# Optimization experiments

Hardware: AMD Instinct MI355X
Metric: run time of the kernel (lower is better)

## Reference

```python
import jax, jax.numpy as jnp
import numpy as np

N = 262144          # batch size
C = 100             # num_classes
R0, R1 = 0.95, 1.0  # recall_range
LAM = 0.5           # lambda_pauc
LS = 0.1            # label_smoothing
MAX_PAUC = R1 - R0


def setup_inputs() -> dict:
    key = jax.random.key(0)
    k1, k2 = jax.random.split(key)
    predictions = jax.random.normal(k1, (N, C), dtype=jnp.float32)
    targets = jax.random.randint(k2, (N,), 0, C)
    weight = jnp.ones((C,), dtype=jnp.float32)
    return {"predictions": predictions, "targets": targets, "weight": weight}


def _roc_curves(scores, labels):
    """Vectorized per-class ROC. scores, labels: [C, N].
    Replaces the O(N^2) per-threshold loop with sort + cumsum (tie-correct:
    tp at threshold s_j counts ALL samples with score >= s_j)."""
    order = jnp.argsort(-scores, axis=1)                      # descending
    ss = jnp.take_along_axis(scores, order, axis=1)           # [C, N]
    sl = jnp.take_along_axis(labels, order, axis=1)           # [C, N]
    cpos = jnp.cumsum(sl, axis=1)                             # cumulative positives
    # last index within each tie-group of equal scores
    neg = -ss  # ascending
    idx = jax.vmap(lambda a: jnp.searchsorted(a, a, side='right'))(neg) - 1
    tp = jnp.take_along_axis(cpos, idx, axis=1)
    cnt = (idx + 1).astype(scores.dtype)
    fp = cnt - tp
    P = cpos[:, -1:]                       # total positives per class
    Nn = scores.shape[1] - P               # total negatives per class
    tpr = jnp.where(P > 0, tp / jnp.maximum(P, 1.0), 0.0)
    fpr = jnp.where(Nn > 0, fp / jnp.maximum(Nn, 1.0), 0.0)
    return fpr, tpr


def reference(predictions, targets, weight):
    probs = jax.nn.softmax(predictions, axis=1)               # [N, C]
    onehot = jnp.eye(C, dtype=predictions.dtype)[targets]     # [N, C]
    onehot_s = (1.0 - LS) * onehot + LS / C

    # per-class binary labels (smoothed true-class value > 0.5)
    labels = (onehot_s > 0.5).astype(predictions.dtype).T     # [C, N]
    scores = probs.T                                          # [C, N]

    fpr, tpr = _roc_curves(scores, labels)
    mask = (tpr >= R0) & (tpr <= R1)
    y = jnp.maximum(tpr - R0, 0.0)
    # tpr is monotone non-decreasing, so the recall mask is contiguous and
    # trapz over the masked subset == sum over adjacent pairs both in mask.
    pm = (mask[:, :-1] & mask[:, 1:]).astype(predictions.dtype)
    pauc = jnp.sum(0.5 * (y[:, :-1] + y[:, 1:]) * (fpr[:, 1:] - fpr[:, :-1]) * pm, axis=1)  # [C]

    avg_p_auc = jnp.sum(pauc * weight) / (jnp.sum(weight) * MAX_PAUC)
    # torch computes TP/FP via .item(): the pAUC path carries no gradient
    avg_p_auc = jax.lax.stop_gradient(jnp.clip(avg_p_auc, 0.0, 1.0))

    log_probs = jax.nn.log_softmax(predictions, axis=1)
    ce_loss = -jnp.mean(jnp.sum(onehot_s * log_probs * weight, axis=1))
    pauc_loss = 1.0 - avg_p_auc ** 2
    return (1.0 - LAM) * ce_loss + LAM * pauc_loss
```

## Files before the change

### kernel.cpp

```cpp
#include <hip/hip_runtime.h>
#include <math.h>

#define WAVE 64
constexpr int   CC      = 100;
constexpr int   MAXM    = 160;
constexpr int   BUCKET  = 4096;
constexpr int   USTRIDE = 161;
constexpr int   LCAP    = 2048;
constexpr float LSMOOTH = 0.1f;
constexpr int   TILE    = 64;
constexpr int   T4TILE  = TILE * CC / 4;
constexpr int   K3AGRID = 1024;
constexpr int   K3BGRID = 128;

__device__ __forceinline__ void gload_lds16(const void* g, void* lds) {
    __builtin_amdgcn_global_load_lds(
        (const __attribute__((address_space(1))) void*)g,
        (__attribute__((address_space(3))) void*)lds, 16, 0, 0);
}

__global__ __launch_bounds__(256) void k1_tile(
    const float* __restrict__ pred, const int* __restrict__ targets,
    const float* __restrict__ weight, float* __restrict__ L_out,
    float* __restrict__ pos_out, float* __restrict__ ce_partial, int N)
{
    __shared__ float tile[TILE * CC];
    __shared__ int   ttgt[TILE];
    __shared__ float tL[TILE], tpos[TILE];
    __shared__ float cered[4];
    const int tid = threadIdx.x;
    const int r0  = blockIdx.x * TILE;

    const float4* src = (const float4*)(pred + (size_t)r0 * CC);
    {
        int t = tid;
        #pragma unroll
        for (int k = 0; k < T4TILE / 256; ++k) {
            gload_lds16((const void*)(src + t), (char*)tile + (size_t)t * 16);
            t += 256;
        }
        if (t < T4TILE)
            gload_lds16((const void*)(src + t), (char*)tile + (size_t)t * 16);
    }
    if (tid < TILE) ttgt[tid] = targets[r0 + tid];
    asm volatile("s_waitcnt vmcnt(0)" ::: "memory");
    __syncthreads();

    const int x = tid & 15;
    const int G = tid >> 4;
    float w[7];
    #pragma unroll
    for (int j = 0; j < 7; ++j) {
        int c = x + 16 * j;
        w[j] = (c < CC) ? weight[c] : 0.0f;
    }
    float Wl = 0.0f;
    #pragma unroll
    for (int j = 0; j < 7; ++j) Wl += w[j];
    #pragma unroll
    for (int off = 1; off < 16; off <<= 1) Wl += __shfl_xor(Wl, off, 16);

    float ce_acc = 0.0f;
    #pragma unroll
    for (int rr = 0; rr < 4; ++rr) {
        const int r = G * 4 + rr;
        const float* rp = tile + r * CC;
        float v[7];
        #pragma unroll
        for (int j = 0; j < 7; ++j) {
            int c = x + 16 * j;
            v[j] = (c < CC) ? rp[c] : -INFINITY;
        }
        float vmax = v[0];
        #pragma unroll
        for (int j = 1; j < 7; ++j) vmax = fmaxf(vmax, v[j]);
        #pragma unroll
        for (int off = 1; off < 16; off <<= 1) vmax = fmaxf(vmax, __shfl_xor(vmax, off, 16));
        float z = 0.0f, ws = 0.0f;
        #pragma unroll
        for (int j = 0; j < 7; ++j) {
            int c = x + 16 * j;
            if (c < CC) { z += __expf(v[j] - vmax); ws += w[j] * v[j]; }
        }
        #pragma unroll
        for (int off = 1; off < 16; off <<= 1) {
            z  += __shfl_xor(z,  off, 16);
            ws += __shfl_xor(ws, off, 16);
        }
        float L = vmax + __logf(z);
        if (x == 0) {
            int t = ttgt[r];
            float pt = rp[t];
            tL[r] = L; tpos[r] = pt - L;
            ce_acc += -((1.0f - LSMOOTH) * weight[t] * (pt - L)
                        + (LSMOOTH / CC) * (ws - Wl * L));
        }
    }
    #pragma unroll
    for (int off = 32; off; off >>= 1) ce_acc += __shfl_xor(ce_acc, off, WAVE);
    if ((tid & 63) == 0) cered[tid >> 6] = ce_acc;
    __syncthreads();
    if (tid < TILE) {
        L_out[r0 + tid]   = tL[tid];
        pos_out[r0 + tid] = tpos[tid];
    }
    if (tid == 0)
        ce_partial[blockIdx.x] = cered[0] + cered[1] + cered[2] + cered[3];
}

__global__ __launch_bounds__(256) void k1b_scatter(
    const int* __restrict__ targets, const float* __restrict__ pos,
    int* __restrict__ cls_cnt, float* __restrict__ bucket, int N)
{
    __shared__ int hist[CC];
    __shared__ int base[CC];
    __shared__ int loc[CC];
    const int tid = threadIdx.x;
    const int rowsPerBlock = N / gridDim.x;
    const int r0 = blockIdx.x * rowsPerBlock;
    const int r1 = r0 + rowsPerBlock;
    for (int c = tid; c < CC; c += blockDim.x) { hist[c] = 0; loc[c] = 0; }
    __syncthreads();
    for (int r = r0 + tid; r < r1; r += blockDim.x)
        atomicAdd(&hist[targets[r]], 1);
    __syncthreads();
    for (int c = tid; c < CC; c += blockDim.x)
        base[c] = (hist[c] > 0) ? atomicAdd(&cls_cnt[c], hist[c]) : 0;
    __syncthreads();
    for (int r = r0 + tid; r < r1; r += blockDim.x) {
        int c = targets[r];
        int idx = base[c] + atomicAdd(&loc[c], 1);
        if (idx < BUCKET) bucket[(size_t)c * BUCKET + idx] = pos[r];
    }
}

__global__ __launch_bounds__(256) void k2_select(
    const float* __restrict__ bucket, const int* __restrict__ cls_cnt,
    float* __restrict__ u, int* __restrict__ m_arr, int* __restrict__ P_arr,
    float* __restrict__ wm_arr)
{
    __shared__ unsigned int keys[BUCKET];
    __shared__ unsigned int hist[256];
    __shared__ unsigned int scan[256];
    __shared__ unsigned int sel[256];
    __shared__ unsigned int s_prefix;
    __shared__ int s_rank;
    __shared__ int cnt_lt;
    const int c   = blockIdx.x;
    const int tid = threadIdx.x;
    const int P = min(cls_cnt[c], BUCKET);
    double Kd = 0.95 * (double)P;
    int kf = (int)floor(Kd);
    int m = P - kf;
    if (m > MAXM) m = MAXM;
    if (m < 0) m = 0;
    if (tid == 0) {
        m_arr[c] = m; P_arr[c] = P;
        wm_arr[c] = (float)((double)(kf + 1) - Kd);
        s_prefix = 0; s_rank = m - 1; cnt_lt = 0;
    }
    for (int i = tid; i < P; i += 256) {
        unsigned int b = __float_as_uint(bucket[(size_t)c * BUCKET + i]);
        keys[i] = (b & 0x80000000u) ? ~b : (b | 0x80000000u);
    }
    __syncthreads();
    if (m == 0) return;

    for (int shift = 24; shift >= 0; shift -= 8) {
        hist[tid] = 0;
        __syncthreads();
        unsigned int pref = s_prefix;
        for (int i = tid; i < P; i += 256) {
            unsigned int k = keys[i];
            bool match = (shift == 24) || ((k >> (shift + 8)) == pref);
            if (match) atomicAdd(&hist[(k >> shift) & 255u], 1u);
        }
        __syncthreads();
        if (tid < 64) {
            unsigned h0 = hist[tid*4], h1 = hist[tid*4+1],
                     h2 = hist[tid*4+2], h3 = hist[tid*4+3];
            unsigned s0 = h0, s1 = s0 + h1, s2 = s1 + h2, s3 = s2 + h3;
            unsigned sc = s3;
            #pragma unroll
            for (int off = 1; off < 64; off <<= 1) {
                unsigned t2 = __shfl_up(sc, (unsigned)off, 64);
                if (tid >= off) sc += t2;
            }
            unsigned excl = sc - s3;
            scan[tid*4]   = excl + s0;
            scan[tid*4+1] = excl + s1;
            scan[tid*4+2] = excl + s2;
            scan[tid*4+3] = excl + s3;
        }
        __syncthreads();
        int r = s_rank;
        unsigned int inc = scan[tid];
        unsigned int exc = inc - hist[tid];
        __syncthreads();
        if ((unsigned int)r >= exc && (unsigned int)r < inc) {
            s_rank   = r - (int)exc;
            s_prefix = (pref << 8) | (unsigned int)tid;
        }
        __syncthreads();
    }
    const unsigned int kth = s_prefix;

    for (int i = tid; i < P; i += 256) {
        unsigned int k = keys[i];
        if (k < kth) {
            int pslot = atomicAdd(&cnt_lt, 1);
            sel[pslot] = k;
        }
    }
    __syncthreads();
    const int nlt = cnt_lt;
    for (int j = nlt + tid; j < 256; j += 256) sel[j] = (j < m) ? kth : 0xFFFFFFFFu;
    __syncthreads();
    for (int kk = 2; kk <= 256; kk <<= 1) {
        for (int j = kk >> 1; j > 0; j >>= 1) {
            int i = tid, ixj = tid ^ j;
            if (ixj > i) {
                unsigned int a = sel[i], b = sel[ixj];
                bool up = ((i & kk) == 0);
                if ((a > b) == up) { sel[i] = b; sel[ixj] = a; }
            }
            __syncthreads();
        }
    }
    if (tid < m) {
        unsigned int k = sel[tid];
        unsigned int b = (k & 0x80000000u) ? (k & 0x7fffffffu) : ~k;
        u[c * MAXM + tid] = __uint_as_float(b);
    }
}

__device__ __forceinline__ int ubound(const float* uc, int m, float key, int maxidx) {
    int l = 0;
    #pragma unroll
    for (int s = 128; s; s >>= 1) {
        int p = l + s - 1;
        float val = uc[p < maxidx ? p : maxidx];
        l += ((p < m) && (val <= key)) ? s : 0;
    }
    return l;
}

__global__ __launch_bounds__(256) void k3a_stream(
    const float4* __restrict__ pred4, const float* __restrict__ L,
    const float* __restrict__ u, const int* __restrict__ m_arr,
    uint2* __restrict__ list, int* __restrict__ list_cnt, int list_cap,
    unsigned long long* __restrict__ g_pack, int total4)
{
    __shared__ float umax_s[CC];
    __shared__ uint2 buf[LCAP];
    __shared__ int lcnt;
    __shared__ int gbase;
    const int tid = threadIdx.x;
    if (tid < CC) {
        int m = m_arr[tid];
        umax_s[tid] = (m > 0) ? u[tid * MAXM + m - 1] : -INFINITY;
    }
    if (tid == 0) lcnt = 0;
    __syncthreads();

    auto proc = [&](float4 v, float Ln, int j) {
        float4 um = *((const float4*)&umax_s[j * 4]);
        float s0 = v.x - Ln, s1 = v.y - Ln, s2 = v.z - Ln, s3 = v.w - Ln;
        #pragma unroll
        for (int q = 0; q < 4; ++q) {
            float scv = (q == 0) ? s0 : (q == 1) ? s1 : (q == 2) ? s2 : s3;
            float mx  = (q == 0) ? um.x : (q == 1) ? um.y : (q == 2) ? um.z : um.w;
            if (scv < mx) {
                int c = j * 4 + q;
                int idx = atomicAdd(&lcnt, 1);
                if (idx < LCAP) {
                    buf[idx] = make_uint2((unsigned int)c, __float_as_uint(scv));
                } else {
                    int m = m_arr[c];
                    int l = ubound(u + c * MAXM, m, scv, MAXM - 1);
                    atomicAdd(&g_pack[c],
                        (1ull << 32) | (unsigned long long)(unsigned)(m - 1 - l));
                }
            }
        }
    };

    const int stride = K3AGRID * 256;
    int i = blockIdx.x * 256 + tid;
    while (i < total4) {
        int i2 = i + stride;
        bool has2 = (i2 < total4);
        float4 v0 = pred4[i];
        float4 v1 = has2 ? pred4[i2] : make_float4(0.f, 0.f, 0.f, 0.f);
        int n0 = i / 25, j0 = i - n0 * 25;
        float L0 = L[n0];
        proc(v0, L0, j0);
        if (has2) {
            int n1 = i2 / 25, j1 = i2 - n1 * 25;
            proc(v1, L[n1], j1);
        }
        i += 2 * stride;
    }
    __syncthreads();
    int cnt = min(lcnt, LCAP);
    if (tid == 0) gbase = atomicAdd(list_cnt, cnt);
    __syncthreads();
    const int base0 = gbase;
    for (int k = tid; k < cnt; k += 256) {
        int gi = base0 + k;
        if (gi < list_cap) {
            list[gi] = buf[k];
        } else {
            uint2 e = buf[k];
            int c = (int)e.x; float scv = __uint_as_float(e.y);
            int m = m_arr[c];
            int l = ubound(u + c * MAXM, m, scv, MAXM - 1);
            atomicAdd(&g_pack[c],
                (1ull << 32) | (unsigned long long)(unsigned)(m - 1 - l));
        }
    }
}

__global__ __launch_bounds__(256) void k3b_rank(
    const uint2* __restrict__ list, const int* __restrict__ list_cnt, int list_cap,
    const float* __restrict__ u, const int* __restrict__ m_arr,
    unsigned long long* __restrict__ g_pack)
{
    __shared__ float us[CC * USTRIDE];
    __shared__ int sm[CC];
    __shared__ unsigned long long lpack[CC];
    const int tid = threadIdx.x;
    for (int c = tid; c < CC; c += 256) { sm[c] = m_arr[c]; lpack[c] = 0ull; }
    for (int t = tid; t < CC * MAXM; t += 256) {
        int c = t / MAXM, k = t - c * MAXM;
        us[c * USTRIDE + k] = u[t];
    }
    __syncthreads();
    const int n = min(*list_cnt, list_cap);
    const int stride = K3BGRID * 256;
    for (int base = blockIdx.x * 256 + tid; base < n; base += 8 * stride) {
        int bb8[8]; int mm8[8]; float kk8[8]; bool hh8[8]; int cc8[8];
        #pragma unroll
        for (int t = 0; t < 8; ++t) {
            int idx = base + t * stride;
            bool h = idx < n;
            uint2 e = h ? list[idx] : make_uint2(0u, 0u);
            hh8[t] = h;
            cc8[t] = (int)e.x;
            bb8[t] = (int)e.x * USTRIDE;
            mm8[t] = h ? sm[(int)e.x] : 0;
            kk8[t] = __uint_as_float(e.y);
        }
        int ll8[8] = {0, 0, 0, 0, 0, 0, 0, 0};
        #pragma unroll
        for (int s = 128; s; s >>= 1) {
            #pragma unroll
            for (int t = 0; t < 8; ++t) {
                int p = ll8[t] + s - 1;
                float val = us[bb8[t] + (p < USTRIDE - 1 ? p : USTRIDE - 1)];
                ll8[t] += ((p < mm8[t]) && (val <= kk8[t])) ? s : 0;
            }
        }
        #pragma unroll
        for (int t = 0; t < 8; ++t)
            if (hh8[t]) {
                unsigned long long pk =
                    (1ull << 32) | (unsigned long long)(unsigned)(mm8[t] - 1 - ll8[t]);
                atomicAdd(&lpack[cc8[t]], pk);
            }
    }
    __syncthreads();
    for (int c = tid; c < CC; c += 256) {
        unsigned long long pk = lpack[c];
        if (pk) atomicAdd(&g_pack[c], pk);
    }
}

__global__ __launch_bounds__(256) void k4_final(
    const float* __restrict__ ce_partial, int nPartial,
    const float* __restrict__ weight, const int* __restrict__ P_arr,
    const int* __restrict__ m_arr, const float* __restrict__ wm_arr,
    const unsigned long long* __restrict__ g_pack,
    float* __restrict__ out, int N)
{
    __shared__ double r1[256], r2[256], r3[256];
    double ce = 0.0;
    for (int i = threadIdx.x; i < nPartial; i += blockDim.x) ce += (double)ce_partial[i];
    double p = 0.0, wsum = 0.0;
    for (int c = threadIdx.x; c < CC; c += blockDim.x) {
        int P = P_arr[c], m = m_arr[c];
        double wgt = (double)weight[c];
        long long Nn = (long long)N - P;
        if (P > 0 && Nn > 0 && m > 0) {
            unsigned long long pk = g_pack[c];
            int gc = (int)(pk >> 32);
            int gs = (int)(pk & 0xffffffffull);
            double wm = (double)wm_arr[c];
            double S   = (double)gs + wm * (double)gc;
            double sub = 0.5 * (double)(m - 1) * (double)(m - 2) + wm * (double)(m - 1);
            double pc  = (S - sub) / ((double)Nn * (double)P);
            if (pc < 0.0) pc = 0.0;
            p += pc * wgt;
        }
        wsum += wgt;
    }
    r1[threadIdx.x] = ce; r2[threadIdx.x] = p; r3[threadIdx.x] = wsum;
    __syncthreads();
    for (int off = blockDim.x >> 1; off; off >>= 1) {
        if ((int)threadIdx.x < off) {
            r1[threadIdx.x] += r1[threadIdx.x + off];
            r2[threadIdx.x] += r2[threadIdx.x + off];
            r3[threadIdx.x] += r3[threadIdx.x + off];
        }
        __syncthreads();
    }
    if (threadIdx.x == 0) {
        double ce_loss = r1[0] / (double)N;
        double avg = r2[0] / (r3[0] * 0.05);
        avg = fmin(fmax(avg, 0.0), 1.0);
        out[0] = (float)(0.5 * ce_loss + 0.5 * (1.0 - avg * avg));
    }
}

extern "C" void kernel_launch(void* const* d_in, const int* in_sizes, int n_in,
                              void* d_out, int out_size, void* d_ws, size_t ws_size,
                              hipStream_t stream) {
    (void)n_in; (void)out_size;
    const float* pred    = (const float*)d_in[0];
    const int*   targets = (const int*)d_in[1];
    const float* weight  = (const float*)d_in[2];
    float* out = (float*)d_out;
    const int N = in_sizes[1];

    const int K1_BLOCKS = N / TILE;
    char* base = (char*)d_ws;
    size_t off = 0;
    auto take = [&](size_t bytes) { char* q = base + off; off += (bytes + 15) & ~(size_t)15; return q; };
    float* L_ws       = (float*)take((size_t)N * 4);
    float* pos_ws     = (float*)take((size_t)N * 4);
    float* ce_partial = (float*)take((size_t)K1_BLOCKS * 4);
    float* u          = (float*)take((size_t)CC * MAXM * 4);
    int*   m_arr      = (int*)take(CC * 4);
    int*   P_arr      = (int*)take(CC * 4);
    float* wm_arr     = (float*)take(CC * 4);
    int*   zero_blk   = (int*)take(304 * 4);
    int*   cls_cnt  = zero_blk;
    unsigned long long* g_pack = (unsigned long long*)(zero_blk + CC);
    int*   list_cnt = zero_blk + 3 * CC;
    float* bucket     = (float*)take((size_t)CC * BUCKET * 4);
    uint2* list       = (uint2*)(base + off);
    long long rem     = (long long)ws_size - (long long)off;
    int list_cap      = (rem > 0) ? (int)(rem / 8) : 0;

    hipMemsetAsync(zero_blk, 0, 304 * 4, stream);

    k1_tile<<<K1_BLOCKS, 256, 0, stream>>>(pred, targets, weight, L_ws, pos_ws,
                                           ce_partial, N);
    k1b_scatter<<<256, 256, 0, stream>>>(targets, pos_ws, cls_cnt, bucket, N);
    k2_select<<<CC, 256, 0, stream>>>(bucket, cls_cnt, u, m_arr, P_arr, wm_arr);
    const int total4 = (int)((size_t)N * CC / 4);
    k3a_stream<<<K3AGRID, 256, 0, stream>>>((const float4*)pred, L_ws, u, m_arr,
                                            list, list_cnt, list_cap, g_pack, total4);
    k3b_rank<<<K3BGRID, 256, 0, stream>>>(list, list_cnt, list_cap, u, m_arr, g_pack);
    k4_final<<<1, 256, 0, stream>>>(ce_partial, K1_BLOCKS, weight, P_arr, m_arr, wm_arr,
                                    g_pack, out, N);
}
```

Before: 266.5 us.

## Replace per-class binary search with coarse LDS splitter scan plus global fine scan

The rank kernel no longer stages the full per-class threshold array in LDS. It now keeps only every eighth element as coarse splitters in a small padded LDS table, counts splitters at or below the key with a linear scan, then reads the eight-element chunk from global memory as two float4 loads to finish the count. The grid grows from 128 to 1024 blocks and the per-thread batch shrinks to 6. This cuts LDS staging per block so the larger grid can launch cheaply, at the cost of a linear scan over all coarse splitters and extra global gathers per element. The coarse-plus-fine counting relies on the thresholds being sorted ascending.

```diff
diff --git a/kernel.cpp b/kernel.cpp
--- a/kernel.cpp
+++ b/kernel.cpp
@@ -5,13 +5,15 @@
 constexpr int   CC      = 100;
 constexpr int   MAXM    = 160;
 constexpr int   BUCKET  = 4096;
-constexpr int   USTRIDE = 161;
 constexpr int   LCAP    = 2048;
 constexpr float LSMOOTH = 0.1f;
 constexpr int   TILE    = 64;
 constexpr int   T4TILE  = TILE * CC / 4;
 constexpr int   K3AGRID = 1024;
-constexpr int   K3BGRID = 128;
+constexpr int   K3BGRID = 1024;
+constexpr int   G8      = MAXM / 8;
+constexpr int   UCSTRIDE= 23;
+constexpr int   BATCH   = 6;
 
 __device__ __forceinline__ void gload_lds16(const void* g, void* lds) {
     __builtin_amdgcn_global_load_lds(
@@ -326,48 +328,67 @@
     const float* __restrict__ u, const int* __restrict__ m_arr,
     unsigned long long* __restrict__ g_pack)
 {
-    __shared__ float us[CC * USTRIDE];
+    __shared__ float uc[CC * UCSTRIDE];
     __shared__ int sm[CC];
     __shared__ unsigned long long lpack[CC];
     const int tid = threadIdx.x;
     for (int c = tid; c < CC; c += 256) { sm[c] = m_arr[c]; lpack[c] = 0ull; }
-    for (int t = tid; t < CC * MAXM; t += 256) {
-        int c = t / MAXM, k = t - c * MAXM;
-        us[c * USTRIDE + k] = u[t];
+    for (int t = tid; t < CC * G8; t += 256) {
+        int c = t / G8, g = t - c * G8;
+        int j = g * 8 + 7;
+        uc[c * UCSTRIDE + g] = (j < m_arr[c]) ? u[c * MAXM + j] : INFINITY;
     }
     __syncthreads();
     const int n = min(*list_cnt, list_cap);
     const int stride = K3BGRID * 256;
-    for (int base = blockIdx.x * 256 + tid; base < n; base += 8 * stride) {
-        int bb8[8]; int mm8[8]; float kk8[8]; bool hh8[8]; int cc8[8];
-        #pragma unroll
-        for (int t = 0; t < 8; ++t) {
+    for (int base = blockIdx.x * 256 + tid; base < n; base += BATCH * stride) {
+        bool hh[BATCH]; int cc[BATCH], mm[BATCH], bb[BATCH]; float kk[BATCH];
+        #pragma unroll
+        for (int t = 0; t < BATCH; ++t) {
             int idx = base + t * stride;
             bool h = idx < n;
             uint2 e = h ? list[idx] : make_uint2(0u, 0u);
-            hh8[t] = h;
-            cc8[t] = (int)e.x;
-            bb8[t] = (int)e.x * USTRIDE;
-            mm8[t] = h ? sm[(int)e.x] : 0;
-            kk8[t] = __uint_as_float(e.y);
-        }
-        int ll8[8] = {0, 0, 0, 0, 0, 0, 0, 0};
-        #pragma unroll
-        for (int s = 128; s; s >>= 1) {
+            hh[t] = h;
+            cc[t] = (int)e.x;
+            mm[t] = sm[(int)e.x];
+            kk[t] = __uint_as_float(e.y);
+            bb[t] = 0;
+        }
+        #pragma unroll
+        for (int g = 0; g < G8; ++g) {
             #pragma unroll
-            for (int t = 0; t < 8; ++t) {
-                int p = ll8[t] + s - 1;
-                float val = us[bb8[t] + (p < USTRIDE - 1 ? p : USTRIDE - 1)];
-                ll8[t] += ((p < mm8[t]) && (val <= kk8[t])) ? s : 0;
+            for (int t = 0; t < BATCH; ++t)
+                bb[t] += (uc[cc[t] * UCSTRIDE + g] <= kk[t]) ? 1 : 0;
+        }
+        float4 fa[BATCH], fb[BATCH];
+        int fbase[BATCH];
+        #pragma unroll
+        for (int t = 0; t < BATCH; ++t) {
+            int fo = 8 * bb[t];
+            if (fo > MAXM - 8) fo = MAXM - 8;
+            fbase[t] = fo;
+            const float4* fp = (const float4*)(u + (size_t)cc[t] * MAXM + fo);
+            fa[t] = fp[0]; fb[t] = fp[1];
+        }
+        #pragma unroll
+        for (int t = 0; t < BATCH; ++t) {
+            if (hh[t]) {
+                int m2 = mm[t], fo = fbase[t];
+                float key = kk[t];
+                int l = fo;
+                l += (fo + 0 < m2 && fa[t].x <= key) ? 1 : 0;
+                l += (fo + 1 < m2 && fa[t].y <= key) ? 1 : 0;
+                l += (fo + 2 < m2 && fa[t].z <= key) ? 1 : 0;
+                l += (fo + 3 < m2 && fa[t].w <= key) ? 1 : 0;
+                l += (fo + 4 < m2 && fb[t].x <= key) ? 1 : 0;
+                l += (fo + 5 < m2 && fb[t].y <= key) ? 1 : 0;
+                l += (fo + 6 < m2 && fb[t].z <= key) ? 1 : 0;
+                l += (fo + 7 < m2 && fb[t].w <= key) ? 1 : 0;
+                unsigned long long pk =
+                    (1ull << 32) | (unsigned long long)(unsigned)(m2 - 1 - l);
+                atomicAdd(&lpack[cc[t]], pk);
             }
         }
-        #pragma unroll
-        for (int t = 0; t < 8; ++t)
-            if (hh8[t]) {
-                unsigned long long pk =
-                    (1ull << 32) | (unsigned long long)(unsigned)(mm8[t] - 1 - ll8[t]);
-                atomicAdd(&lpack[cc8[t]], pk);
-            }
     }
     __syncthreads();
     for (int c = tid; c < CC; c += 256) {
```

Result: faster. 260.7 us (-2.2%).

## Fuse scatter+select via grid barrier, fold finalize into rank kernel, drop memset

Applied to the files above, without the earlier changes.

Zeroes the counter block inside the first kernel instead of issuing a separate memset. Merges the per-class scatter and top-m selection kernels with a software grid barrier, and folds the final reduction into the rank kernel using a last-block-done counter. The rank kernel's grid also grows from 128 to 512 blocks. The aim is to cut kernel launches and inter-kernel gaps. The grid barrier relies on all 256 blocks being co-resident, and the larger rank grid raises the number of atomic flushes.

```diff
diff --git a/kernel.cpp b/kernel.cpp
--- a/kernel.cpp
+++ b/kernel.cpp
@@ -10,8 +10,10 @@
 constexpr float LSMOOTH = 0.1f;
 constexpr int   TILE    = 64;
 constexpr int   T4TILE  = TILE * CC / 4;
+constexpr int   K12GRID = 256;
 constexpr int   K3AGRID = 1024;
-constexpr int   K3BGRID = 128;
+constexpr int   K3BGRID = 512;
+constexpr int   ZBLKN   = 304;
 
 __device__ __forceinline__ void gload_lds16(const void* g, void* lds) {
     __builtin_amdgcn_global_load_lds(
@@ -19,10 +21,22 @@
         (__attribute__((address_space(3))) void*)lds, 16, 0, 0);
 }
 
+__device__ __forceinline__ void grid_barrier(int* bar, int nblk) {
+    __threadfence();
+    __syncthreads();
+    if (threadIdx.x == 0) {
+        atomicAdd(bar, 1);
+        while (__hip_atomic_load(bar, __ATOMIC_ACQUIRE, __HIP_MEMORY_SCOPE_AGENT) < nblk)
+            __builtin_amdgcn_s_sleep(2);
+    }
+    __syncthreads();
+}
+
 __global__ __launch_bounds__(256) void k1_tile(
     const float* __restrict__ pred, const int* __restrict__ targets,
     const float* __restrict__ weight, float* __restrict__ L_out,
-    float* __restrict__ pos_out, float* __restrict__ ce_partial, int N)
+    float* __restrict__ pos_out, float* __restrict__ ce_partial,
+    int* __restrict__ zb, int N)
 {
     __shared__ float tile[TILE * CC];
     __shared__ int   ttgt[TILE];
@@ -42,6 +56,8 @@
         if (t < T4TILE)
             gload_lds16((const void*)(src + t), (char*)tile + (size_t)t * 16);
     }
+    if (blockIdx.x == 0)
+        for (int t = tid; t < ZBLKN; t += 256) zb[t] = 0;
     if (tid < TILE) ttgt[tid] = targets[r0 + tid];
     asm volatile("s_waitcnt vmcnt(0)" ::: "memory");
     __syncthreads();
@@ -108,46 +124,45 @@
         ce_partial[blockIdx.x] = cered[0] + cered[1] + cered[2] + cered[3];
 }
 
-__global__ __launch_bounds__(256) void k1b_scatter(
+struct K12A { int hist[CC]; int base[CC]; int loc[CC]; };
+struct K12B {
+    unsigned int keys[BUCKET];
+    unsigned int hist[256], scan[256], sel[256];
+    unsigned int prefix; int rank; int cnt_lt;
+};
+union K12U { K12A a; K12B b; };
+
+__global__ __launch_bounds__(256) void k1b_k2(
     const int* __restrict__ targets, const float* __restrict__ pos,
-    int* __restrict__ cls_cnt, float* __restrict__ bucket, int N)
+    int* __restrict__ cls_cnt, float* __restrict__ bucket,
+    float* __restrict__ u, int* __restrict__ m_arr, int* __restrict__ P_arr,
+    float* __restrict__ wm_arr, int* __restrict__ bar, int N)
 {
-    __shared__ int hist[CC];
-    __shared__ int base[CC];
-    __shared__ int loc[CC];
+    __shared__ K12U sh;
     const int tid = threadIdx.x;
-    const int rowsPerBlock = N / gridDim.x;
-    const int r0 = blockIdx.x * rowsPerBlock;
-    const int r1 = r0 + rowsPerBlock;
-    for (int c = tid; c < CC; c += blockDim.x) { hist[c] = 0; loc[c] = 0; }
-    __syncthreads();
-    for (int r = r0 + tid; r < r1; r += blockDim.x)
-        atomicAdd(&hist[targets[r]], 1);
-    __syncthreads();
-    for (int c = tid; c < CC; c += blockDim.x)
-        base[c] = (hist[c] > 0) ? atomicAdd(&cls_cnt[c], hist[c]) : 0;
-    __syncthreads();
-    for (int r = r0 + tid; r < r1; r += blockDim.x) {
-        int c = targets[r];
-        int idx = base[c] + atomicAdd(&loc[c], 1);
-        if (idx < BUCKET) bucket[(size_t)c * BUCKET + idx] = pos[r];
-    }
-}
-
-__global__ __launch_bounds__(256) void k2_select(
-    const float* __restrict__ bucket, const int* __restrict__ cls_cnt,
-    float* __restrict__ u, int* __restrict__ m_arr, int* __restrict__ P_arr,
-    float* __restrict__ wm_arr)
-{
-    __shared__ unsigned int keys[BUCKET];
-    __shared__ unsigned int hist[256];
-    __shared__ unsigned int scan[256];
-    __shared__ unsigned int sel[256];
-    __shared__ unsigned int s_prefix;
-    __shared__ int s_rank;
-    __shared__ int cnt_lt;
-    const int c   = blockIdx.x;
-    const int tid = threadIdx.x;
+
+    {
+        const int rowsPerBlock = N / K12GRID;
+        const int r0 = blockIdx.x * rowsPerBlock;
+        const int r1 = r0 + rowsPerBlock;
+        for (int c = tid; c < CC; c += 256) { sh.a.hist[c] = 0; sh.a.loc[c] = 0; }
+        __syncthreads();
+        for (int r = r0 + tid; r < r1; r += 256)
+            atomicAdd(&sh.a.hist[targets[r]], 1);
+        __syncthreads();
+        for (int c = tid; c < CC; c += 256)
+            sh.a.base[c] = (sh.a.hist[c] > 0) ? atomicAdd(&cls_cnt[c], sh.a.hist[c]) : 0;
+        __syncthreads();
+        for (int r = r0 + tid; r < r1; r += 256) {
+            int c = targets[r];
+            int idx = sh.a.base[c] + atomicAdd(&sh.a.loc[c], 1);
+            if (idx < BUCKET) bucket[(size_t)c * BUCKET + idx] = pos[r];
+        }
+    }
+    grid_barrier(bar, K12GRID);
+
+    if (blockIdx.x >= CC) return;
+    const int c = blockIdx.x;
     const int P = min(cls_cnt[c], BUCKET);
     double Kd = 0.95 * (double)P;
     int kf = (int)floor(Kd);
@@ -157,28 +172,29 @@
     if (tid == 0) {
         m_arr[c] = m; P_arr[c] = P;
         wm_arr[c] = (float)((double)(kf + 1) - Kd);
-        s_prefix = 0; s_rank = m - 1; cnt_lt = 0;
-    }
+        sh.b.prefix = 0; sh.b.rank = m - 1; sh.b.cnt_lt = 0;
+    }
+    __syncthreads();
     for (int i = tid; i < P; i += 256) {
-        unsigned int b = __float_as_uint(bucket[(size_t)c * BUCKET + i]);
-        keys[i] = (b & 0x80000000u) ? ~b : (b | 0x80000000u);
+        unsigned int bb = __float_as_uint(bucket[(size_t)c * BUCKET + i]);
+        sh.b.keys[i] = (bb & 0x80000000u) ? ~bb : (bb | 0x80000000u);
     }
     __syncthreads();
     if (m == 0) return;
 
     for (int shift = 24; shift >= 0; shift -= 8) {
-        hist[tid] = 0;
-        __syncthreads();
-        unsigned int pref = s_prefix;
+        sh.b.hist[tid] = 0;
+        __syncthreads();
+        unsigned int pref = sh.b.prefix;
         for (int i = tid; i < P; i += 256) {
-            unsigned int k = keys[i];
+            unsigned int k = sh.b.keys[i];
             bool match = (shift == 24) || ((k >> (shift + 8)) == pref);
-            if (match) atomicAdd(&hist[(k >> shift) & 255u], 1u);
+            if (match) atomicAdd(&sh.b.hist[(k >> shift) & 255u], 1u);
         }
         __syncthreads();
         if (tid < 64) {
-            unsigned h0 = hist[tid*4], h1 = hist[tid*4+1],
-                     h2 = hist[tid*4+2], h3 = hist[tid*4+3];
+            unsigned h0 = sh.b.hist[tid*4], h1 = sh.b.hist[tid*4+1],
+                     h2 = sh.b.hist[tid*4+2], h3 = sh.b.hist[tid*4+3];
             unsigned s0 = h0, s1 = s0 + h1, s2 = s1 + h2, s3 = s2 + h3;
             unsigned sc = s3;
             #pragma unroll
@@ -187,50 +203,50 @@
                 if (tid >= off) sc += t2;
             }
             unsigned excl = sc - s3;
-            scan[tid*4]   = excl + s0;
-            scan[tid*4+1] = excl + s1;
-            scan[tid*4+2] = excl + s2;
-            scan[tid*4+3] = excl + s3;
-        }
-        __syncthreads();
-        int r = s_rank;
-        unsigned int inc = scan[tid];
-        unsigned int exc = inc - hist[tid];
+            sh.b.scan[tid*4]   = excl + s0;
+            sh.b.scan[tid*4+1] = excl + s1;
+            sh.b.scan[tid*4+2] = excl + s2;
+            sh.b.scan[tid*4+3] = excl + s3;
+        }
+        __syncthreads();
+        int r = sh.b.rank;
+        unsigned int inc = sh.b.scan[tid];
+        unsigned int exc = inc - sh.b.hist[tid];
         __syncthreads();
         if ((unsigned int)r >= exc && (unsigned int)r < inc) {
-            s_rank   = r - (int)exc;
-            s_prefix = (pref << 8) | (unsigned int)tid;
-        }
-        __syncthreads();
-    }
-    const unsigned int kth = s_prefix;
+            sh.b.rank   = r - (int)exc;
+            sh.b.prefix = (pref << 8) | (unsigned int)tid;
+        }
+        __syncthreads();
+    }
+    const unsigned int kth = sh.b.prefix;
 
     for (int i = tid; i < P; i += 256) {
-        unsigned int k = keys[i];
+        unsigned int k = sh.b.keys[i];
         if (k < kth) {
-            int pslot = atomicAdd(&cnt_lt, 1);
-            sel[pslot] = k;
-        }
-    }
-    __syncthreads();
-    const int nlt = cnt_lt;
-    for (int j = nlt + tid; j < 256; j += 256) sel[j] = (j < m) ? kth : 0xFFFFFFFFu;
+            int pslot = atomicAdd(&sh.b.cnt_lt, 1);
+            sh.b.sel[pslot] = k;
+        }
+    }
+    __syncthreads();
+    const int nlt = sh.b.cnt_lt;
+    for (int j = nlt + tid; j < 256; j += 256) sh.b.sel[j] = (j < m) ? kth : 0xFFFFFFFFu;
     __syncthreads();
     for (int kk = 2; kk <= 256; kk <<= 1) {
         for (int j = kk >> 1; j > 0; j >>= 1) {
             int i = tid, ixj = tid ^ j;
             if (ixj > i) {
-                unsigned int a = sel[i], b = sel[ixj];
+                unsigned int a = sh.b.sel[i], bb = sh.b.sel[ixj];
                 bool up = ((i & kk) == 0);
-                if ((a > b) == up) { sel[i] = b; sel[ixj] = a; }
+                if ((a > bb) == up) { sh.b.sel[i] = bb; sh.b.sel[ixj] = a; }
             }
             __syncthreads();
         }
     }
     if (tid < m) {
-        unsigned int k = sel[tid];
-        unsigned int b = (k & 0x80000000u) ? (k & 0x7fffffffu) : ~k;
-        u[c * MAXM + tid] = __uint_as_float(b);
+        unsigned int k = sh.b.sel[tid];
+        unsigned int bb = (k & 0x80000000u) ? (k & 0x7fffffffu) : ~k;
+        u[c * MAXM + tid] = __uint_as_float(bb);
     }
 }
 
@@ -321,14 +337,19 @@
     }
 }
 
-__global__ __launch_bounds__(256) void k3b_rank(
+__global__ __launch_bounds__(256) void k3b_k4(
     const uint2* __restrict__ list, const int* __restrict__ list_cnt, int list_cap,
     const float* __restrict__ u, const int* __restrict__ m_arr,
-    unsigned long long* __restrict__ g_pack)
+    unsigned long long* __restrict__ g_pack, int* __restrict__ done,
+    const float* __restrict__ ce_partial, int nPartial,
+    const float* __restrict__ weight, const int* __restrict__ P_arr,
+    const float* __restrict__ wm_arr, float* __restrict__ out, int N)
 {
     __shared__ float us[CC * USTRIDE];
     __shared__ int sm[CC];
     __shared__ unsigned long long lpack[CC];
+    __shared__ int lastflag;
+    __shared__ double r1[256], r2[256], r3[256];
     const int tid = threadIdx.x;
     for (int c = tid; c < CC; c += 256) { sm[c] = m_arr[c]; lpack[c] = 0ull; }
     for (int t = tid; t < CC * MAXM; t += 256) {
@@ -374,25 +395,25 @@
         unsigned long long pk = lpack[c];
         if (pk) atomicAdd(&g_pack[c], pk);
     }
-}
-
-__global__ __launch_bounds__(256) void k4_final(
-    const float* __restrict__ ce_partial, int nPartial,
-    const float* __restrict__ weight, const int* __restrict__ P_arr,
-    const int* __restrict__ m_arr, const float* __restrict__ wm_arr,
-    const unsigned long long* __restrict__ g_pack,
-    float* __restrict__ out, int N)
-{
-    __shared__ double r1[256], r2[256], r3[256];
+    __threadfence();
+    __syncthreads();
+    if (tid == 0) {
+        int r = atomicAdd(done, 1);
+        lastflag = (r == (int)gridDim.x - 1) ? 1 : 0;
+    }
+    __syncthreads();
+    if (!lastflag) return;
+
     double ce = 0.0;
-    for (int i = threadIdx.x; i < nPartial; i += blockDim.x) ce += (double)ce_partial[i];
+    for (int t = tid; t < nPartial; t += 256) ce += (double)ce_partial[t];
     double p = 0.0, wsum = 0.0;
-    for (int c = threadIdx.x; c < CC; c += blockDim.x) {
-        int P = P_arr[c], m = m_arr[c];
+    for (int c = tid; c < CC; c += 256) {
+        int P = P_arr[c], m = sm[c];
         double wgt = (double)weight[c];
         long long Nn = (long long)N - P;
         if (P > 0 && Nn > 0 && m > 0) {
-            unsigned long long pk = g_pack[c];
+            unsigned long long pk = __hip_atomic_load(&g_pack[c], __ATOMIC_RELAXED,
+                                                      __HIP_MEMORY_SCOPE_AGENT);
             int gc = (int)(pk >> 32);
             int gs = (int)(pk & 0xffffffffull);
             double wm = (double)wm_arr[c];
@@ -404,17 +425,17 @@
         }
         wsum += wgt;
     }
-    r1[threadIdx.x] = ce; r2[threadIdx.x] = p; r3[threadIdx.x] = wsum;
-    __syncthreads();
-    for (int off = blockDim.x >> 1; off; off >>= 1) {
-        if ((int)threadIdx.x < off) {
-            r1[threadIdx.x] += r1[threadIdx.x + off];
-            r2[threadIdx.x] += r2[threadIdx.x + off];
-            r3[threadIdx.x] += r3[threadIdx.x + off];
-        }
-        __syncthreads();
-    }
-    if (threadIdx.x == 0) {
+    r1[tid] = ce; r2[tid] = p; r3[tid] = wsum;
+    __syncthreads();
+    for (int off = 128; off; off >>= 1) {
+        if (tid < off) {
+            r1[tid] += r1[tid + off];
+            r2[tid] += r2[tid + off];
+            r3[tid] += r3[tid + off];
+        }
+        __syncthreads();
+    }
+    if (tid == 0) {
         double ce_loss = r1[0] / (double)N;
         double avg = r2[0] / (r3[0] * 0.05);
         avg = fmin(fmax(avg, 0.0), 1.0);
@@ -443,25 +464,25 @@
     int*   m_arr      = (int*)take(CC * 4);
     int*   P_arr      = (int*)take(CC * 4);
     float* wm_arr     = (float*)take(CC * 4);
-    int*   zero_blk   = (int*)take(304 * 4);
+    int*   zero_blk   = (int*)take(ZBLKN * 4);
     int*   cls_cnt  = zero_blk;
     unsigned long long* g_pack = (unsigned long long*)(zero_blk + CC);
     int*   list_cnt = zero_blk + 3 * CC;
+    int*   done     = zero_blk + 3 * CC + 1;
+    int*   bar      = zero_blk + 3 * CC + 2;
     float* bucket     = (float*)take((size_t)CC * BUCKET * 4);
     uint2* list       = (uint2*)(base + off);
     long long rem     = (long long)ws_size - (long long)off;
     int list_cap      = (rem > 0) ? (int)(rem / 8) : 0;
 
-    hipMemsetAsync(zero_blk, 0, 304 * 4, stream);
-
     k1_tile<<<K1_BLOCKS, 256, 0, stream>>>(pred, targets, weight, L_ws, pos_ws,
-                                           ce_partial, N);
-    k1b_scatter<<<256, 256, 0, stream>>>(targets, pos_ws, cls_cnt, bucket, N);
-    k2_select<<<CC, 256, 0, stream>>>(bucket, cls_cnt, u, m_arr, P_arr, wm_arr);
+                                           ce_partial, zero_blk, N);
+    k1b_k2<<<K12GRID, 256, 0, stream>>>(targets, pos_ws, cls_cnt, bucket,
+                                        u, m_arr, P_arr, wm_arr, bar, N);
     const int total4 = (int)((size_t)N * CC / 4);
     k3a_stream<<<K3AGRID, 256, 0, stream>>>((const float4*)pred, L_ws, u, m_arr,
                                             list, list_cnt, list_cap, g_pack, total4);
-    k3b_rank<<<K3BGRID, 256, 0, stream>>>(list, list_cnt, list_cap, u, m_arr, g_pack);
-    k4_final<<<1, 256, 0, stream>>>(ce_partial, K1_BLOCKS, weight, P_arr, m_arr, wm_arr,
-                                    g_pack, out, N);
-}
+    k3b_k4<<<K3BGRID, 256, 0, stream>>>(list, list_cnt, list_cap, u, m_arr, g_pack,
+                                        done, ce_partial, K1_BLOCKS, weight, P_arr,
+                                        wm_arr, out, N);
+}
```

New measurement: 319.3 us. 1.2x slower.
